# Performance work log

Hardware: AMD Instinct MI355X
Metric: run time of the kernel (lower is better)

## Reference

```python
import jax, jax.numpy as jnp
import numpy as np

B, OBS, E, H, NT, A, NH = 65536, 128, 64, 128, 7, 16, 4
HD = E // NH  # head dim = 16


def setup_inputs() -> dict:
    key = jax.random.key(0)
    ks = jax.random.split(key, 16)
    def p(i, shape, s=0.05):
        return jax.random.normal(ks[i], shape, jnp.float32) * s
    return {
        "obs": jax.random.normal(ks[0], (B, OBS), jnp.float32),
        "prev_belief": jax.random.normal(ks[1], (B, H), jnp.float32),
        "teammate_hidden": jax.random.normal(ks[2], (B, NT, H), jnp.float32),
        # obs_encoder: Linear(OBS->E), ReLU, Linear(E->E), ReLU
        "W1": p(3, (E, OBS)), "b1": jnp.zeros((E,), jnp.float32),
        "W2": p(4, (E, E)), "b2": jnp.zeros((E,), jnp.float32),
        # hidden_proj: Linear(H->E)
        "Wp": p(5, (E, H)), "bp": jnp.zeros((E,), jnp.float32),
        # nn.MultiheadAttention packed in-proj + out-proj
        "in_proj_w": p(6, (3 * E, E)), "in_proj_b": jnp.zeros((3 * E,), jnp.float32),
        "out_proj_w": p(7, (E, E)), "out_proj_b": jnp.zeros((E,), jnp.float32),
        # GRUCell(input=2E, hidden=H): gate order r, z, n (torch convention)
        "gru_wih": p(8, (3 * H, 2 * E)), "gru_whh": p(9, (3 * H, H)),
        "gru_bih": jnp.zeros((3 * H,), jnp.float32), "gru_bhh": jnp.zeros((3 * H,), jnp.float32),
        # policy head (gain 0.01 init -> small scale)
        "Wpol": p(10, (A, H), 0.01), "bpol": jnp.zeros((A,), jnp.float32),
    }


def reference(obs, prev_belief, teammate_hidden,
              W1, b1, W2, b2, Wp, bp,
              in_proj_w, in_proj_b, out_proj_w, out_proj_b,
              gru_wih, gru_whh, gru_bih, gru_bhh, Wpol, bpol):
    # 1. observation encoder (2-layer ReLU MLP)
    h_obs = jax.nn.relu(jax.nn.relu(obs @ W1.T + b1) @ W2.T + b2)          # [B,E]
    # 2-3. project own belief (query) and teammate hiddens (keys/values)
    q_in = prev_belief @ Wp.T + bp                                          # [B,E]
    kv_in = teammate_hidden @ Wp.T + bp                                     # [B,NT,E]
    # 4. multi-head attention (query len 1 over NT teammates), torch MHA semantics
    Wq, Wk, Wv = jnp.split(in_proj_w, 3, axis=0)
    bq, bk, bv = jnp.split(in_proj_b, 3, axis=0)
    q = (q_in @ Wq.T + bq).reshape(B, NH, HD)                               # [B,NH,HD]
    k = (kv_in @ Wk.T + bk).reshape(B, NT, NH, HD)                          # [B,NT,NH,HD]
    v = (kv_in @ Wv.T + bv).reshape(B, NT, NH, HD)
    scores = jnp.einsum('bhd,bthd->bht', q, k) / np.float32(np.sqrt(HD))    # [B,NH,NT]
    attn = jax.nn.softmax(scores, axis=-1)
    ctx = jnp.einsum('bht,bthd->bhd', attn, v).reshape(B, E)                # concat heads
    context = ctx @ out_proj_w.T + out_proj_b                               # [B,E]
    attn_weights = attn.mean(axis=1)                                        # avg over heads -> [B,NT]
    # 5. GRUCell update on [h_obs || context]
    x = jnp.concatenate([h_obs, context], axis=-1)                          # [B,2E]
    gi = x @ gru_wih.T + gru_bih
    gh = prev_belief @ gru_whh.T + gru_bhh
    ir, iz, inn = jnp.split(gi, 3, axis=-1)
    hr, hz, hn = jnp.split(gh, 3, axis=-1)
    r = jax.nn.sigmoid(ir + hr)
    z = jax.nn.sigmoid(iz + hz)
    n = jnp.tanh(inn + r * hn)
    belief = (1.0 - z) * n + z * prev_belief                                # [B,H]
    # 6. policy head
    action_logits = belief @ Wpol.T + bpol                                  # [B,A]
    return action_logits, belief, attn_weights
```

## Files before the change

kernel.cpp:

```cpp
#include <hip/hip_runtime.h>

#define DEVINL __device__ __forceinline__

typedef unsigned short u16;
typedef unsigned long long u64;
typedef __attribute__((ext_vector_type(8))) short bf16x8;
typedef __attribute__((ext_vector_type(16))) float f32x16;

#define NB   65536
#define OBSD 128
#define ED   64
#define HD_  128
#define NT   7
#define NA   16

#define OFF_W1   0
#define OFF_W2   8192
#define OFF_WQP  12288
#define OFF_WKP  20480
#define OFF_WVP  28672
#define OFF_WIH  36864
#define OFF_WHH  86016
#define OFF_POL  135168
#define W_TOTAL  137216
#define NBIAS    576

DEVINL u16 f2bf(float f) {
  unsigned u = __float_as_uint(f);
  u += 0x7fff + ((u >> 16) & 1);
  return (u16)(u >> 16);
}
DEVINL float bf2f(u16 h) { return __uint_as_float(((unsigned)h) << 16); }

DEVINL f32x16 mfma(bf16x8 a, bf16x8 b, f32x16 c) {
  return __builtin_amdgcn_mfma_f32_32x32x16_bf16(a, b, c, 0, 0, 0);
}
DEVINL f32x16 zero16() {
  f32x16 z;
#pragma unroll
  for (int i = 0; i < 16; ++i) z[i] = 0.f;
  return z;
}

DEVINL bf16x8 ldsA(const u16* p) {
  union { bf16x8 v; u64 u[2]; } t;
  t.u[0] = *(const u64*)p;
  t.u[1] = *(const u64*)(p + 4);
  return t.v;
}

template<int KS>
DEVINL f32x16 gemm_acc(const u16* __restrict__ bufA, int S, int aRow, int khalf,
                       const u16* __restrict__ wRow, f32x16 acc) {
  const u16* ap = bufA + aRow * S + khalf;
  const u16* bp = wRow + khalf;
#pragma unroll
  for (int ks = 0; ks < KS; ++ks) {
    bf16x8 a = ldsA(ap + ks * 16);
    bf16x8 b = *(const bf16x8*)(bp + ks * 16);
    acc = mfma(a, b, acc);
  }
  return acc;
}

DEVINL void epiLDS(const f32x16& acc, float bias, int rowOff, int col,
                   u16* buf, int S, bool relu) {
#pragma unroll
  for (int r = 0; r < 16; ++r) {
    int row = rowOff + (r & 3) + 8 * (r >> 2);
    float v = acc[r] + bias;
    if (relu) v = fmaxf(v, 0.f);
    buf[row * S + col] = f2bf(v);
  }
}

DEVINL void rd16(const u16* p, float* o) {
  union { u64 u[4]; u16 s[16]; } t;
  t.u[0] = ((const u64*)p)[0]; t.u[1] = ((const u64*)p)[1];
  t.u[2] = ((const u64*)p)[2]; t.u[3] = ((const u64*)p)[3];
#pragma unroll
  for (int d = 0; d < 16; ++d) o[d] = bf2f(t.s[d]);
}

DEVINL float sigf(float x) { return 1.f / (1.f + __expf(-x)); }

__global__ void prep_weights(const float* __restrict__ W1, const float* __restrict__ W2,
                             const float* __restrict__ Wp, const float* __restrict__ bp,
                             const float* __restrict__ inpw, const float* __restrict__ inpb,
                             const float* __restrict__ outpw, const float* __restrict__ outpb,
                             const float* __restrict__ wih, const float* __restrict__ bih,
                             const float* __restrict__ whh, const float* __restrict__ wpol,
                             u16* __restrict__ ws) {
  int i = blockIdx.x * 256 + threadIdx.x;
  if (i < W_TOTAL) {
    float v;
    if (i < OFF_W2)       v = W1[i];
    else if (i < OFF_WQP) v = W2[i - OFF_W2];
    else if (i < OFF_WIH) {
      int o = i - OFF_WQP;
      int mat = o >> 13;
      int e = (o >> 7) & 63;
      int h = o & 127;
      const float* wr = inpw + (mat * 64 + e) * 64;
      float acc = 0.f;
#pragma unroll 4
      for (int c = 0; c < 64; ++c) acc += wr[c] * Wp[c * 128 + h];
      v = (mat == 0) ? acc * 0.25f : acc;
    } else if (i < OFF_WHH) {
      int o = i - OFF_WIH;
      int g = o >> 7, c = o & 127;
      if (c < 64) v = wih[g * 128 + c];
      else {
        int d = c - 64;
        float acc = 0.f;
#pragma unroll 4
        for (int c2 = 0; c2 < 64; ++c2) acc += wih[g * 128 + 64 + c2] * outpw[c2 * 64 + d];
        v = acc;
      }
    }
    else if (i < OFF_POL) v = whh[i - OFF_WHH];
    else                  v = wpol[i - OFF_POL];
    ws[i] = f2bf(v);
  } else if (i < W_TOTAL + NBIAS) {
    float* wsF = (float*)(ws + W_TOTAL);
    int o = i - W_TOTAL;
    float acc = 0.f;
    if (o < 192) {
      int mat = o >> 6, e = o & 63;
      const float* wr = inpw + (mat * 64 + e) * 64;
      for (int c = 0; c < 64; ++c) acc += wr[c] * bp[c];
      acc += inpb[mat * 64 + e];
      if (mat == 0) acc *= 0.25f;
    } else {
      int g = o - 192;
      for (int c = 0; c < 64; ++c) acc += wih[g * 128 + 64 + c] * outpb[c];
      acc += bih[g];
    }
    wsF[o] = acc;
  }
}

__global__ __launch_bounds__(256, 2)
void aerial_main(const float* __restrict__ obs, const float* __restrict__ pb,
                 const float* __restrict__ th,
                 const float* __restrict__ b1, const float* __restrict__ b2,
                 const float* __restrict__ bpol, const float* __restrict__ bhh,
                 const u16* __restrict__ wsb,
                 float* __restrict__ outLog, float* __restrict__ outBel,
                 float* __restrict__ outAttn) {
  __shared__ u16 bufP[64 * 132];
  __shared__ u16 bufB[64 * 132];
  __shared__ u16 bufH1[64 * 68];
  __shared__ u16 bufHO[64 * 68];
  __shared__ u16 bufQ[64 * 68];

  const int tid   = threadIdx.x;
  const int lane  = tid & 63;
  const int m     = lane & 31;
  const int half  = lane >> 5;
  const int khalf = half * 8;
  const int wv    = tid >> 6;
  const int mt    = wv & 1;
  const int nh    = wv >> 1;
  const int aRow  = 32 * mt + m;
  const int rowOff = 32 * mt + 4 * half;
  const int col64 = nh * 32 + m;
  const int gRow0 = blockIdx.x * 64;

  const float* wsF = (const float*)(wsb + W_TOTAL);

  auto stage = [&](const float* src, int srcStride, u16* dst) {
#pragma unroll
    for (int i = 0; i < 8; ++i) {
      int f4 = tid + i * 256;
      int row = f4 >> 5;
      int c4  = f4 & 31;
      float4 v = *(const float4*)(src + (size_t)row * srcStride + c4 * 4);
      ushort4 o;
      o.x = f2bf(v.x); o.y = f2bf(v.y); o.z = f2bf(v.z); o.w = f2bf(v.w);
      *(ushort4*)(dst + row * 132 + c4 * 4) = o;
    }
  };

  stage(obs + (size_t)gRow0 * OBSD, OBSD, bufB);
  stage(pb  + (size_t)gRow0 * HD_,  HD_,  bufP);
  __syncthreads();

  {
    f32x16 acc = gemm_acc<8>(bufB, 132, aRow, khalf, wsb + OFF_W1 + col64 * 128, zero16());
    epiLDS(acc, b1[col64], rowOff, col64, bufH1, 68, true);
  }
  {
    f32x16 acc = gemm_acc<8>(bufP, 132, aRow, khalf, wsb + OFF_WQP + col64 * 128, zero16());
    epiLDS(acc, wsF[col64], rowOff, col64, bufQ, 68, false);
  }
  __syncthreads();

  {
    f32x16 acc = gemm_acc<4>(bufH1, 68, aRow, khalf, wsb + OFF_W2 + col64 * 64, zero16());
    epiLDS(acc, b2[col64], rowOff, col64, bufHO, 68, true);
  }
  const int b  = tid >> 2;
  const int hh = tid & 3;
  float qreg[16];
  rd16(bufQ + b * 68 + hh * 16, qreg);

  const u16* bKp = wsb + OFF_WKP + col64 * 128 + khalf;
  const u16* bVp = wsb + OFF_WVP + col64 * 128 + khalf;
  const float bkF = wsF[64 + col64];
  const float bvF = wsF[128 + col64];
  float ctx[16];
#pragma unroll
  for (int d = 0; d < 16; ++d) ctx[d] = 0.f;
  float l = 0.f, parr[NT];

#pragma unroll
  for (int t = 0; t < NT; ++t) {
    stage(th + (size_t)gRow0 * (NT * HD_) + t * HD_, NT * HD_, bufB);
    __syncthreads();
    {
      bf16x8 af[8];
#pragma unroll
      for (int ks = 0; ks < 8; ++ks) af[ks] = ldsA(bufB + aRow * 132 + ks * 16 + khalf);
      f32x16 aK = zero16(), aV = zero16();
#pragma unroll
      for (int ks = 0; ks < 8; ++ks) {
        aK = mfma(af[ks], *(const bf16x8*)(bKp + ks * 16), aK);
        aV = mfma(af[ks], *(const bf16x8*)(bVp + ks * 16), aV);
      }
      epiLDS(aK, bkF, rowOff, col64, bufQ, 68, false);
      epiLDS(aV, bvF, rowOff, col64, bufH1, 68, false);
    }
    __syncthreads();
    {
      float kv[16];
      rd16(bufQ + b * 68 + hh * 16, kv);
      float s = 0.f;
#pragma unroll
      for (int d = 0; d < 16; ++d) s += qreg[d] * kv[d];
      float p = __expf(s);
      l += p; parr[t] = p;
      rd16(bufH1 + b * 68 + hh * 16, kv);
#pragma unroll
      for (int d = 0; d < 16; ++d) ctx[d] += p * kv[d];
    }
  }

  {
    float linv = 1.f / l;
#pragma unroll
    for (int t = 0; t < NT; ++t) {
      float a = parr[t] * linv;
      a += __shfl_xor(a, 1);
      a += __shfl_xor(a, 2);
      if (hh == 0) outAttn[(size_t)(gRow0 + b) * NT + t] = a * 0.25f;
    }
#pragma unroll
    for (int d = 0; d < 16; ++d) bufH1[b * 68 + hh * 16 + d] = f2bf(ctx[d] * linv);
  }
  __syncthreads();

  bf16x8 ax[8], apb[8];
#pragma unroll
  for (int ks = 0; ks < 4; ++ks) ax[ks]     = ldsA(bufHO + aRow * 68 + ks * 16 + khalf);
#pragma unroll
  for (int ks = 0; ks < 4; ++ks) ax[4 + ks] = ldsA(bufH1 + aRow * 68 + ks * 16 + khalf);
#pragma unroll
  for (int ks = 0; ks < 8; ++ks) apb[ks]    = ldsA(bufP  + aRow * 132 + ks * 16 + khalf);

#pragma unroll
  for (int hj = 0; hj < 2; ++hj) {
    int j = nh * 32 + hj * 64 + m;
    const u16* wr = wsb + OFF_WIH + (size_t)(0 * HD_ + j) * 128;
    const u16* wz = wsb + OFF_WIH + (size_t)(1 * HD_ + j) * 128;
    const u16* wn = wsb + OFF_WIH + (size_t)(2 * HD_ + j) * 128;
    const u16* vr = wsb + OFF_WHH + (size_t)(0 * HD_ + j) * 128;
    const u16* vz = wsb + OFF_WHH + (size_t)(1 * HD_ + j) * 128;
    const u16* vn = wsb + OFF_WHH + (size_t)(2 * HD_ + j) * 128;
    f32x16 ar = zero16(), az = zero16(), ai = zero16(), ah = zero16();
#pragma unroll
    for (int ks = 0; ks < 8; ++ks) {
      int ko = ks * 16 + khalf;
      ar = mfma(ax[ks], *(const bf16x8*)(wr + ko), ar);
      az = mfma(ax[ks], *(const bf16x8*)(wz + ko), az);
      ai = mfma(ax[ks], *(const bf16x8*)(wn + ko), ai);
    }
#pragma unroll
    for (int ks = 0; ks < 8; ++ks) {
      int ko = ks * 16 + khalf;
      ar = mfma(apb[ks], *(const bf16x8*)(vr + ko), ar);
      az = mfma(apb[ks], *(const bf16x8*)(vz + ko), az);
      ah = mfma(apb[ks], *(const bf16x8*)(vn + ko), ah);
    }
    float br_ = wsF[192 + j] + bhh[j];
    float bz_ = wsF[192 + 128 + j] + bhh[128 + j];
    float bi_ = wsF[192 + 256 + j];
    float bh_ = bhh[256 + j];
#pragma unroll
    for (int r = 0; r < 16; ++r) {
      int row = rowOff + (r & 3) + 8 * (r >> 2);
      float rr = sigf(ar[r] + br_);
      float zz = sigf(az[r] + bz_);
      float xn = ai[r] + bi_ + rr * (ah[r] + bh_);
      xn = fminf(fmaxf(xn, -15.f), 15.f);
      float tt = __expf(2.f * xn);
      float nn = (tt - 1.f) / (tt + 1.f);
      float pv = bf2f(bufP[row * 132 + j]);
      float bel = (1.f - zz) * nn + zz * pv;
      outBel[(size_t)(gRow0 + row) * HD_ + j] = bel;
      bufB[row * 132 + j] = f2bf(bel);
    }
  }
  __syncthreads();

  if (nh == 0) {
    int nclamp = (m < 16) ? m : 15;
    f32x16 acc = gemm_acc<8>(bufB, 132, aRow, khalf, wsb + OFF_POL + nclamp * 128, zero16());
    if (m < 16) {
      float bv = bpol[m];
#pragma unroll
      for (int r = 0; r < 16; ++r) {
        int row = rowOff + (r & 3) + 8 * (r >> 2);
        outLog[(size_t)(gRow0 + row) * NA + m] = acc[r] + bv;
      }
    }
  }
}

extern "C" void kernel_launch(void* const* d_in, const int* in_sizes, int n_in,
                              void* d_out, int out_size, void* d_ws, size_t ws_size,
                              hipStream_t stream) {
  const float* obs   = (const float*)d_in[0];
  const float* pb    = (const float*)d_in[1];
  const float* th    = (const float*)d_in[2];
  const float* W1    = (const float*)d_in[3];
  const float* b1    = (const float*)d_in[4];
  const float* W2    = (const float*)d_in[5];
  const float* b2    = (const float*)d_in[6];
  const float* Wp    = (const float*)d_in[7];
  const float* bp    = (const float*)d_in[8];
  const float* inpw  = (const float*)d_in[9];
  const float* inpb  = (const float*)d_in[10];
  const float* outpw = (const float*)d_in[11];
  const float* outpb = (const float*)d_in[12];
  const float* wih   = (const float*)d_in[13];
  const float* whh   = (const float*)d_in[14];
  const float* bih   = (const float*)d_in[15];
  const float* bhh   = (const float*)d_in[16];
  const float* wpol  = (const float*)d_in[17];
  const float* bpol  = (const float*)d_in[18];

  u16* wsb = (u16*)d_ws;
  float* outLog  = (float*)d_out;
  float* outBel  = outLog + (size_t)NB * NA;
  float* outAttn = outBel + (size_t)NB * HD_;

  prep_weights<<<(W_TOTAL + NBIAS + 255) / 256, 256, 0, stream>>>(
      W1, W2, Wp, bp, inpw, inpb, outpw, outpb, wih, bih, whh, wpol, wsb);
  aerial_main<<<NB / 64, 256, 0, stream>>>(obs, pb, th, b1, b2, bpol, bhh, wsb,
                                           outLog, outBel, outAttn);
}
```

Measured before the change: 483.9 us.

## Double-buffer teammate hidden tiles with register prefetch across the attention loop

Teammate-hidden rows are now loaded into registers two steps ahead and converted into an alternating pair of LDS buffers. Each step's global load latency is meant to overlap the MFMA and softmax work of earlier steps instead of stalling before every step. This costs an extra 64x132 bf16 LDS buffer and 32 more live registers per thread. With launch bounds of 256 threads and 2 blocks per CU, that could lower occupancy or cause spills.

```diff
diff --git a/kernel.cpp b/kernel.cpp
--- a/kernel.cpp
+++ b/kernel.cpp
@@ -149,7 +149,8 @@
                  float* __restrict__ outLog, float* __restrict__ outBel,
                  float* __restrict__ outAttn) {
   __shared__ u16 bufP[64 * 132];
-  __shared__ u16 bufB[64 * 132];
+  __shared__ u16 bufT0[64 * 132];
+  __shared__ u16 bufT1[64 * 132];
   __shared__ u16 bufH1[64 * 68];
   __shared__ u16 bufHO[64 * 68];
   __shared__ u16 bufQ[64 * 68];
@@ -182,18 +183,41 @@
     }
   };
 
-  stage(obs + (size_t)gRow0 * OBSD, OBSD, bufB);
+  float4 sreg[8];
+  auto issue = [&](int t) {
+#pragma unroll
+    for (int i = 0; i < 8; ++i) {
+      int f4 = tid + i * 256;
+      int row = f4 >> 5, c4 = f4 & 31;
+      sreg[i] = *(const float4*)(th + ((size_t)(gRow0 + row) * NT + t) * HD_ + c4 * 4);
+    }
+  };
+  auto swrite = [&](u16* dst) {
+#pragma unroll
+    for (int i = 0; i < 8; ++i) {
+      int f4 = tid + i * 256;
+      int row = f4 >> 5, c4 = f4 & 31;
+      ushort4 o;
+      o.x = f2bf(sreg[i].x); o.y = f2bf(sreg[i].y);
+      o.z = f2bf(sreg[i].z); o.w = f2bf(sreg[i].w);
+      *(ushort4*)(dst + row * 132 + c4 * 4) = o;
+    }
+  };
+
+  issue(0);
+  stage(obs + (size_t)gRow0 * OBSD, OBSD, bufT0);
   stage(pb  + (size_t)gRow0 * HD_,  HD_,  bufP);
   __syncthreads();
 
   {
-    f32x16 acc = gemm_acc<8>(bufB, 132, aRow, khalf, wsb + OFF_W1 + col64 * 128, zero16());
+    f32x16 acc = gemm_acc<8>(bufT0, 132, aRow, khalf, wsb + OFF_W1 + col64 * 128, zero16());
     epiLDS(acc, b1[col64], rowOff, col64, bufH1, 68, true);
   }
   {
     f32x16 acc = gemm_acc<8>(bufP, 132, aRow, khalf, wsb + OFF_WQP + col64 * 128, zero16());
     epiLDS(acc, wsF[col64], rowOff, col64, bufQ, 68, false);
   }
+  swrite(bufT1);
   __syncthreads();
 
   {
@@ -204,6 +228,7 @@
   const int hh = tid & 3;
   float qreg[16];
   rd16(bufQ + b * 68 + hh * 16, qreg);
+  issue(1);
 
   const u16* bKp = wsb + OFF_WKP + col64 * 128 + khalf;
   const u16* bVp = wsb + OFF_WVP + col64 * 128 + khalf;
@@ -216,12 +241,13 @@
 
 #pragma unroll
   for (int t = 0; t < NT; ++t) {
-    stage(th + (size_t)gRow0 * (NT * HD_) + t * HD_, NT * HD_, bufB);
+    u16* tb = (t & 1) ? bufT0 : bufT1;
+    u16* tbn = (t & 1) ? bufT1 : bufT0;
     __syncthreads();
     {
       bf16x8 af[8];
 #pragma unroll
-      for (int ks = 0; ks < 8; ++ks) af[ks] = ldsA(bufB + aRow * 132 + ks * 16 + khalf);
+      for (int ks = 0; ks < 8; ++ks) af[ks] = ldsA(tb + aRow * 132 + ks * 16 + khalf);
       f32x16 aK = zero16(), aV = zero16();
 #pragma unroll
       for (int ks = 0; ks < 8; ++ks) {
@@ -231,7 +257,9 @@
       epiLDS(aK, bkF, rowOff, col64, bufQ, 68, false);
       epiLDS(aV, bvF, rowOff, col64, bufH1, 68, false);
     }
+    if (t + 1 < NT) swrite(tbn);
     __syncthreads();
+    if (t + 2 < NT) issue(t + 2);
     {
       float kv[16];
       rd16(bufQ + b * 68 + hh * 16, kv);
@@ -308,14 +336,14 @@
       float pv = bf2f(bufP[row * 132 + j]);
       float bel = (1.f - zz) * nn + zz * pv;
       outBel[(size_t)(gRow0 + row) * HD_ + j] = bel;
-      bufB[row * 132 + j] = f2bf(bel);
+      bufT0[row * 132 + j] = f2bf(bel);
     }
   }
   __syncthreads();
 
   if (nh == 0) {
     int nclamp = (m < 16) ? m : 15;
-    f32x16 acc = gemm_acc<8>(bufB, 132, aRow, khalf, wsb + OFF_POL + nclamp * 128, zero16());
+    f32x16 acc = gemm_acc<8>(bufT0, 132, aRow, khalf, wsb + OFF_POL + nclamp * 128, zero16());
     if (m < 16) {
       float bv = bpol[m];
 #pragma unroll
```

After: 483.0 us. About the same (-0.2%).

## Stage weight slabs through LDS and hoist K/V weights into registers

Applied to the files above, without the earlier changes.

Adds a second 64x132 LDS buffer and cooperatively stages the W1 and GRU weight slabs through it, so the MFMA B operands come from LDS rather than from per-lane global bf16x8 loads. The K/V projection weights are loaded into registers once, before the teammate loop, instead of being re-read from global memory on each of the 7 iterations. The cost is extra LDS per block, which may reduce occupancy, more registers for the hoisted fragments, and twelve extra block barriers in the GRU stage.

```diff
diff --git a/kernel.cpp b/kernel.cpp
--- a/kernel.cpp
+++ b/kernel.cpp
@@ -149,7 +149,8 @@
                  float* __restrict__ outLog, float* __restrict__ outBel,
                  float* __restrict__ outAttn) {
   __shared__ u16 bufP[64 * 132];
-  __shared__ u16 bufB[64 * 132];
+  __shared__ u16 bufT[64 * 132];
+  __shared__ u16 bufW[64 * 132];
   __shared__ u16 bufH1[64 * 68];
   __shared__ u16 bufHO[64 * 68];
   __shared__ u16 bufQ[64 * 68];
@@ -182,12 +183,28 @@
     }
   };
 
-  stage(obs + (size_t)gRow0 * OBSD, OBSD, bufB);
+  auto stageW = [&](const u16* src) {
+#pragma unroll
+    for (int i = 0; i < 8; ++i) {
+      int idx = tid + i * 256;
+      int row = idx >> 5;
+      int c   = (idx & 31) * 4;
+      *(u64*)(bufW + row * 132 + c) = *(const u64*)(src + row * 128 + c);
+    }
+  };
+
+  stage(obs + (size_t)gRow0 * OBSD, OBSD, bufT);
   stage(pb  + (size_t)gRow0 * HD_,  HD_,  bufP);
+  stageW(wsb + OFF_W1);
   __syncthreads();
 
   {
-    f32x16 acc = gemm_acc<8>(bufB, 132, aRow, khalf, wsb + OFF_W1 + col64 * 128, zero16());
+    f32x16 acc = zero16();
+    const u16* ap = bufT + aRow * 132 + khalf;
+    const u16* bp = bufW + col64 * 132 + khalf;
+#pragma unroll
+    for (int ks = 0; ks < 8; ++ks)
+      acc = mfma(ldsA(ap + ks * 16), ldsA(bp + ks * 16), acc);
     epiLDS(acc, b1[col64], rowOff, col64, bufH1, 68, true);
   }
   {
@@ -205,8 +222,17 @@
   float qreg[16];
   rd16(bufQ + b * 68 + hh * 16, qreg);
 
-  const u16* bKp = wsb + OFF_WKP + col64 * 128 + khalf;
-  const u16* bVp = wsb + OFF_WVP + col64 * 128 + khalf;
+  bf16x8 wK[8], wV[8];
+  {
+    const u16* bKp = wsb + OFF_WKP + col64 * 128 + khalf;
+    const u16* bVp = wsb + OFF_WVP + col64 * 128 + khalf;
+#pragma unroll
+    for (int ks = 0; ks < 8; ++ks) {
+      wK[ks] = *(const bf16x8*)(bKp + ks * 16);
+      wV[ks] = *(const bf16x8*)(bVp + ks * 16);
+    }
+  }
+
   const float bkF = wsF[64 + col64];
   const float bvF = wsF[128 + col64];
   float ctx[16];
@@ -216,17 +242,17 @@
 
 #pragma unroll
   for (int t = 0; t < NT; ++t) {
-    stage(th + (size_t)gRow0 * (NT * HD_) + t * HD_, NT * HD_, bufB);
+    stage(th + (size_t)gRow0 * (NT * HD_) + t * HD_, NT * HD_, bufT);
     __syncthreads();
     {
       bf16x8 af[8];
 #pragma unroll
-      for (int ks = 0; ks < 8; ++ks) af[ks] = ldsA(bufB + aRow * 132 + ks * 16 + khalf);
+      for (int ks = 0; ks < 8; ++ks) af[ks] = ldsA(bufT + aRow * 132 + ks * 16 + khalf);
       f32x16 aK = zero16(), aV = zero16();
 #pragma unroll
       for (int ks = 0; ks < 8; ++ks) {
-        aK = mfma(af[ks], *(const bf16x8*)(bKp + ks * 16), aK);
-        aV = mfma(af[ks], *(const bf16x8*)(bVp + ks * 16), aV);
+        aK = mfma(af[ks], wK[ks], aK);
+        aV = mfma(af[ks], wV[ks], aV);
       }
       epiLDS(aK, bkF, rowOff, col64, bufQ, 68, false);
       epiLDS(aV, bvF, rowOff, col64, bufH1, 68, false);
@@ -270,28 +296,26 @@
 
 #pragma unroll
   for (int hj = 0; hj < 2; ++hj) {
-    int j = nh * 32 + hj * 64 + m;
-    const u16* wr = wsb + OFF_WIH + (size_t)(0 * HD_ + j) * 128;
-    const u16* wz = wsb + OFF_WIH + (size_t)(1 * HD_ + j) * 128;
-    const u16* wn = wsb + OFF_WIH + (size_t)(2 * HD_ + j) * 128;
-    const u16* vr = wsb + OFF_WHH + (size_t)(0 * HD_ + j) * 128;
-    const u16* vz = wsb + OFF_WHH + (size_t)(1 * HD_ + j) * 128;
-    const u16* vn = wsb + OFF_WHH + (size_t)(2 * HD_ + j) * 128;
     f32x16 ar = zero16(), az = zero16(), ai = zero16(), ah = zero16();
-#pragma unroll
-    for (int ks = 0; ks < 8; ++ks) {
-      int ko = ks * 16 + khalf;
-      ar = mfma(ax[ks], *(const bf16x8*)(wr + ko), ar);
-      az = mfma(ax[ks], *(const bf16x8*)(wz + ko), az);
-      ai = mfma(ax[ks], *(const bf16x8*)(wn + ko), ai);
-    }
-#pragma unroll
-    for (int ks = 0; ks < 8; ++ks) {
-      int ko = ks * 16 + khalf;
-      ar = mfma(apb[ks], *(const bf16x8*)(vr + ko), ar);
-      az = mfma(apb[ks], *(const bf16x8*)(vz + ko), az);
-      ah = mfma(apb[ks], *(const bf16x8*)(vn + ko), ah);
-    }
+    const int wrow = (nh * 32 + m) * 132 + khalf;
+
+#define GRU_SLAB(BASE, FR, ACC)                                             \
+    stageW(wsb + (BASE) + (size_t)hj * 64 * 128);                           \
+    __syncthreads();                                                        \
+    _Pragma("unroll")                                                       \
+    for (int ks = 0; ks < 8; ++ks)                                          \
+      ACC = mfma(FR[ks], ldsA(bufW + wrow + ks * 16), ACC);                 \
+    __syncthreads();
+
+    GRU_SLAB(OFF_WIH + 0 * HD_ * 128, ax,  ar)
+    GRU_SLAB(OFF_WIH + 1 * HD_ * 128, ax,  az)
+    GRU_SLAB(OFF_WIH + 2 * HD_ * 128, ax,  ai)
+    GRU_SLAB(OFF_WHH + 0 * HD_ * 128, apb, ar)
+    GRU_SLAB(OFF_WHH + 1 * HD_ * 128, apb, az)
+    GRU_SLAB(OFF_WHH + 2 * HD_ * 128, apb, ah)
+#undef GRU_SLAB
+
+    int j = hj * 64 + nh * 32 + m;
     float br_ = wsF[192 + j] + bhh[j];
     float bz_ = wsF[192 + 128 + j] + bhh[128 + j];
     float bi_ = wsF[192 + 256 + j];
@@ -308,14 +332,14 @@
       float pv = bf2f(bufP[row * 132 + j]);
       float bel = (1.f - zz) * nn + zz * pv;
       outBel[(size_t)(gRow0 + row) * HD_ + j] = bel;
-      bufB[row * 132 + j] = f2bf(bel);
+      bufT[row * 132 + j] = f2bf(bel);
     }
   }
   __syncthreads();
 
   if (nh == 0) {
     int nclamp = (m < 16) ? m : 15;
-    f32x16 acc = gemm_acc<8>(bufB, 132, aRow, khalf, wsb + OFF_POL + nclamp * 128, zero16());
+    f32x16 acc = gemm_acc<8>(bufT, 132, aRow, khalf, wsb + OFF_POL + nclamp * 128, zero16());
     if (m < 16) {
       float bv = bpol[m];
 #pragma unroll
```

Result: no change. 483.5 us (-0.1%).
